# Optimization experiments

Measured on AMD Instinct MI355X. Metric: run time of the kernel, lower is better.

Reference implementation:

```python
import jax, jax.numpy as jnp
import numpy as np

B, T, D, H = 4, 4096, 1024, 64

def setup_inputs() -> dict:
    key = jax.random.key(0)
    k1, k2, k3, k4 = jax.random.split(key, 4)
    scale = 1.0 / np.sqrt(D)
    return {
        "x": jax.random.normal(k1, (B, T, D), dtype=jnp.float32),
        "Wq": jax.random.normal(k2, (D, H), dtype=jnp.float32) * scale,
        "Wk": jax.random.normal(k3, (D, H), dtype=jnp.float32) * scale,
        "Wv": jax.random.normal(k4, (D, H), dtype=jnp.float32) * scale,
    }

def reference(x, Wq, Wk, Wv):
    # Projections (Linear without bias): [B,T,H]
    q = jnp.einsum('btd,dh->bth', x, Wq)
    k = jnp.einsum('btd,dh->bth', x, Wk)
    v = jnp.einsum('btd,dh->bth', x, Wv)
    head_size = q.shape[-1]
    # Full T x T scores, scaled by sqrt(head_size) as in the source
    attn = jnp.einsum('bqh,bkh->bqk', q, k) / jnp.sqrt(jnp.float32(head_size))
    t = x.shape[1]
    causal = jnp.tril(jnp.ones((t, t), dtype=bool))  # [T,T]
    attn = jnp.where(causal[None, :, :], attn, -jnp.inf)
    attn = jax.nn.softmax(attn, axis=-1)
    # dropout prob = 0.0 -> identity
    out = jnp.einsum('bqk,bkh->bqh', attn, v)
    return out
```

## Files before the change

kernel.cpp:

```cpp
#include <hip/hip_runtime.h>
#include <hip/hip_bf16.h>
#include <math.h>

#define BB 4
#define TT 4096
#define DD 1024
#define HH 64
#define MTOT (BB * TT)
#define NCH 4

typedef short short8 __attribute__((ext_vector_type(8)));
typedef float f32x4  __attribute__((ext_vector_type(4)));
typedef unsigned int u32;
typedef unsigned long long u64;

__device__ __forceinline__ unsigned short f2bf(float f) {
    unsigned u = __builtin_bit_cast(unsigned, f);
    unsigned r = (u + 0x7fffu + ((u >> 16) & 1u)) >> 16;
    return (unsigned short)r;
}

__device__ __forceinline__ unsigned long long pack4(float a, float b, float c, float d) {
    return (unsigned long long)f2bf(a) |
           ((unsigned long long)f2bf(b) << 16) |
           ((unsigned long long)f2bf(c) << 32) |
           ((unsigned long long)f2bf(d) << 48);
}

__device__ __forceinline__ short8 pack8(float4 a, float4 b) {
    short8 r;
    r[0] = (short)f2bf(a.x); r[1] = (short)f2bf(a.y);
    r[2] = (short)f2bf(a.z); r[3] = (short)f2bf(a.w);
    r[4] = (short)f2bf(b.x); r[5] = (short)f2bf(b.y);
    r[6] = (short)f2bf(b.z); r[7] = (short)f2bf(b.w);
    return r;
}

__device__ __forceinline__ void gl16(const void* g, void* l) {
    __builtin_amdgcn_global_load_lds(
        (const __attribute__((address_space(1))) u32*)g,
        (__attribute__((address_space(3))) u32*)l, 16, 0, 0);
}

#define QOFF  0
#define KOFF  (MTOT * HH)
#define VOFF  (2 * MTOT * HH)
#define BF_TOTAL (3 * MTOT * HH)

__global__ __launch_bounds__(256) void transpose_w(
    const float* __restrict__ Wq, const float* __restrict__ Wk,
    const float* __restrict__ Wv, unsigned short* __restrict__ Wt)
{
    const int w = blockIdx.y;
    const float* W = (w == 0) ? Wq : (w == 1) ? Wk : Wv;
    unsigned short* o = Wt + (size_t)w * 64 * 1024;
    const int t  = threadIdx.x;
    const int n4 = t & 15;
    const int k0 = blockIdx.x * 64 + (t >> 4) * 4;

    float v[4][4];
#pragma unroll
    for (int ii = 0; ii < 4; ++ii) {
        float4 r = *(const float4*)&W[(size_t)(k0 + ii) * HH + n4 * 4];
        v[ii][0] = r.x; v[ii][1] = r.y; v[ii][2] = r.z; v[ii][3] = r.w;
    }
#pragma unroll
    for (int cc = 0; cc < 4; ++cc) {
        unsigned long long pk = pack4(v[0][cc], v[1][cc], v[2][cc], v[3][cc]);
        *(unsigned long long*)&o[(size_t)(n4 * 4 + cc) * 1024 + k0] = pk;
    }
}

__global__ __launch_bounds__(256, 2) void qkv_proj(
    const float* __restrict__ x,
    const unsigned short* __restrict__ Wt,
    unsigned short* __restrict__ qkv)
{
    const int tid   = threadIdx.x;
    const int lane  = tid & 63;
    const int wave  = tid >> 6;
    const int l15   = lane & 15;
    const int quad  = lane >> 4;
    const int m0    = blockIdx.x * 32;
    const int strip = wave & 1;
    const int half  = wave >> 1;

    __shared__ float          Af[2][32 * 64];
    __shared__ unsigned short Bs[2][192 * 64];

    const int ar  = lane >> 4;
    const int as  = lane & 15;
    const int bc  = lane >> 3;
    const int bs2 = (lane & 7) ^ bc;

#define STAGEW(it, p)                                                        \
    {                                                                        \
        const int kc_ = (it) * 64;                                           \
        _Pragma("unroll")                                                    \
        for (int jj = 0; jj < 2; ++jj) {                                     \
            int j   = wave * 2 + jj;                                         \
            int row = 4 * j + ar;                                            \
            int sw  = as ^ (row & 15);                                       \
            gl16(x + (size_t)(m0 + row) * DD + kc_ + sw * 4,                 \
                 &Af[p][j * 256]);                                           \
        }                                                                    \
        _Pragma("unroll")                                                    \
        for (int jj = 0; jj < 6; ++jj) {                                     \
            int j    = wave * 6 + jj;                                        \
            int gcol = 8 * j + bc;                                           \
            gl16(Wt + (size_t)gcol * 1024 + kc_ + bs2 * 8,                   \
                 &Bs[p][j * 512]);                                           \
        }                                                                    \
    }

    f32x4 acc[6];
#pragma unroll
    for (int i = 0; i < 6; ++i) acc[i] = (f32x4){0.f, 0.f, 0.f, 0.f};

    STAGEW(0, 0)
    __syncthreads();
    int p = 0;

    for (int it = 0; it < 16; ++it) {
        if (it < 15) STAGEW(it + 1, p ^ 1)

        const int row = strip * 16 + l15;
#pragma unroll
        for (int ks = 0; ks < 2; ++ks) {
            int c0 = ks * 8 + quad * 2;
            float4 a0 = *(const float4*)&Af[p][row * 64 + ((c0)     ^ l15) * 4];
            float4 a1 = *(const float4*)&Af[p][row * 64 + ((c0 + 1) ^ l15) * 4];
            short8 af = pack8(a0, a1);
            int cb = (ks * 4 + quad) ^ (l15 & 7);
#pragma unroll
            for (int jj = 0; jj < 6; ++jj) {
                int col = (half * 6 + jj) * 16 + l15;
                short8 bfr = *(const short8*)&Bs[p][col * 64 + cb * 8];
                acc[jj] = __builtin_amdgcn_mfma_f32_16x16x32_bf16(af, bfr, acc[jj], 0, 0, 0);
            }
        }
        __syncthreads();
        p ^= 1;
    }
#undef STAGEW

    const float QS = 0.125f * 1.44269504088896f;
    unsigned short* q_bf  = qkv + QOFF;
    unsigned short* k_bf  = qkv + KOFF;
    unsigned short* vt_bf = qkv + VOFF;
#pragma unroll
    for (int jj = 0; jj < 6; ++jj) {
        int g = half * 6 + jj, w = g >> 2, col = (g & 3) * 16 + l15;
#pragma unroll
        for (int r = 0; r < 4; ++r) {
            int m = m0 + strip * 16 + quad * 4 + r;
            float val = acc[jj][r];
            if (w == 0) val *= QS;
            unsigned short bv = f2bf(val);
            if (w == 0)      q_bf[(size_t)m * HH + col] = bv;
            else if (w == 1) k_bf[(size_t)m * HH + col] = bv;
            else {
                int b = m >> 12, t = m & 4095;
                vt_bf[(size_t)b * HH * TT + (size_t)col * TT + t] = bv;
            }
        }
    }
}

__global__ __launch_bounds__(256, 3) void flash_attn(
    const unsigned short* __restrict__ qkv,
    float* __restrict__ Opart,
    float* __restrict__ Mpart,
    float* __restrict__ Lpart)
{
    const int qt = 63 - blockIdx.x;
    const int b  = blockIdx.y;
    const int c  = blockIdx.z;
    if (c * 16 > qt) return;
    const int j0   = c * 16;
    const int jmax = min(j0 + 16, qt + 1);

    const int tid  = threadIdx.x;
    const int lane = tid & 63;
    const int wave = tid >> 6;
    const int l15  = lane & 15;
    const int quad = lane >> 4;

    const unsigned short* q_g  = qkv + QOFF + (size_t)b * TT * HH;
    const unsigned short* k_g  = qkv + KOFF + (size_t)b * TT * HH;
    const unsigned short* vt_g = qkv + VOFF + (size_t)b * HH * TT;

    __shared__ unsigned short Ks[2][128 * 64];
    __shared__ unsigned short Vs[64 * 128];

    const int kr3 = lane >> 3;
    const int kch = lane & 7;
    const int vr2 = lane >> 4;
    const int vch = lane & 15;

#define STAGE_K(jr_, p_)                                                      \
    {                                                                         \
        const unsigned short* kp = k_g + (size_t)(jr_) * 64 * HH;             \
        _Pragma("unroll")                                                     \
        for (int i = 0; i < 4; ++i) {                                         \
            int g = wave * 4 + i;                                             \
            gl16(kp + (size_t)(g * 8 + kr3) * HH + (kch ^ kr3) * 8,           \
                 &Ks[p_][g * 512]);                                           \
        }                                                                     \
    }
#define STAGE_V(jr_)                                                          \
    {                                                                         \
        const unsigned short* vp = vt_g + (size_t)(jr_) * 64;                 \
        _Pragma("unroll")                                                     \
        for (int i = 0; i < 4; ++i) {                                         \
            int g = wave * 4 + i;                                             \
            int h = g * 4 + vr2;                                              \
            gl16(vp + (size_t)h * TT + (vch ^ ((h >> 1) & 7)) * 8,            \
                 &Vs[g * 512]);                                               \
        }                                                                     \
    }

    short8 qf[2];
#pragma unroll
    for (int kk = 0; kk < 2; ++kk)
        qf[kk] = *(const short8*)&q_g[(size_t)(qt * 64 + wave * 16 + l15) * HH + kk * 32 + quad * 8];

    f32x4 ov[4];
#pragma unroll
    for (int i = 0; i < 4; ++i) ov[i] = (f32x4){0.f, 0.f, 0.f, 0.f};
    float m_run = -1e30f, l_run = 0.f;

    STAGE_K(j0, 0)
    __syncthreads();
    int p = 0;

    const int swv = 2 * ((l15 >> 1) & 7);

    for (int jr = j0; jr < jmax; jr += 2) {
        const bool two = (jmax - jr) >= 2;

        STAGE_V(jr)
        if (jr + 2 < jmax) STAGE_K(jr + 2, p ^ 1)

        f32x4 st0[4], st1[4];
#pragma unroll
        for (int i = 0; i < 4; ++i) {
            st0[i] = (f32x4){0.f, 0.f, 0.f, 0.f};
            st1[i] = (f32x4){0.f, 0.f, 0.f, 0.f};
        }
#pragma unroll
        for (int kk = 0; kk < 2; ++kk)
#pragma unroll
            for (int mt = 0; mt < 4; ++mt) {
                short8 a = *(const short8*)&Ks[p][(mt * 16 + l15) * 64 +
                                                  (((kk * 4 + quad) ^ (l15 & 7)) * 8)];
                st0[mt] = __builtin_amdgcn_mfma_f32_16x16x32_bf16(a, qf[kk], st0[mt], 0, 0, 0);
            }
        if (two) {
#pragma unroll
            for (int kk = 0; kk < 2; ++kk)
#pragma unroll
                for (int mt = 0; mt < 4; ++mt) {
                    short8 a = *(const short8*)&Ks[p][(64 + mt * 16 + l15) * 64 +
                                                      (((kk * 4 + quad) ^ (l15 & 7)) * 8)];
                    st1[mt] = __builtin_amdgcn_mfma_f32_16x16x32_bf16(a, qf[kk], st1[mt], 0, 0, 0);
                }
        }

        const int qg = wave * 16 + l15;
        if (jr == qt) {
#pragma unroll
            for (int mt = 0; mt < 4; ++mt)
#pragma unroll
                for (int r = 0; r < 4; ++r)
                    if (mt * 16 + quad * 4 + r > qg) st0[mt][r] = -1e30f;
        } else if (two && jr + 1 == qt) {
#pragma unroll
            for (int mt = 0; mt < 4; ++mt)
#pragma unroll
                for (int r = 0; r < 4; ++r)
                    if (mt * 16 + quad * 4 + r > qg) st1[mt][r] = -1e30f;
        }

        float mloc = -1e30f;
#pragma unroll
        for (int mt = 0; mt < 4; ++mt)
#pragma unroll
            for (int r = 0; r < 4; ++r) mloc = fmaxf(mloc, st0[mt][r]);
        if (two) {
#pragma unroll
            for (int mt = 0; mt < 4; ++mt)
#pragma unroll
                for (int r = 0; r < 4; ++r) mloc = fmaxf(mloc, st1[mt][r]);
        }
        mloc = fmaxf(mloc, __shfl_xor(mloc, 16));
        mloc = fmaxf(mloc, __shfl_xor(mloc, 32));
        const float m_new = fmaxf(m_run, mloc);
        const float alpha = exp2f(m_run - m_new);
        m_run = m_new;

        float ssum = 0.f;
#pragma unroll
        for (int mt = 0; mt < 4; ++mt)
#pragma unroll
            for (int r = 0; r < 4; ++r) {
                float pv = exp2f(st0[mt][r] - m_new);
                st0[mt][r] = pv; ssum += pv;
            }
        if (two) {
#pragma unroll
            for (int mt = 0; mt < 4; ++mt)
#pragma unroll
                for (int r = 0; r < 4; ++r) {
                    float pv = exp2f(st1[mt][r] - m_new);
                    st1[mt][r] = pv; ssum += pv;
                }
        }
        ssum += __shfl_xor(ssum, 16);
        ssum += __shfl_xor(ssum, 32);
        l_run = l_run * alpha + ssum;

        short8 pa00, pa01, pa10, pa11;
        {
            u32* pp = (u32*)&pa00;
            asm("v_cvt_pk_bf16_f32 %0, %1, %2" : "=v"(pp[0]) : "v"(st0[0][0]), "v"(st0[0][1]));
            asm("v_cvt_pk_bf16_f32 %0, %1, %2" : "=v"(pp[1]) : "v"(st0[0][2]), "v"(st0[0][3]));
            asm("v_cvt_pk_bf16_f32 %0, %1, %2" : "=v"(pp[2]) : "v"(st0[1][0]), "v"(st0[1][1]));
            asm("v_cvt_pk_bf16_f32 %0, %1, %2" : "=v"(pp[3]) : "v"(st0[1][2]), "v"(st0[1][3]));
            pp = (u32*)&pa01;
            asm("v_cvt_pk_bf16_f32 %0, %1, %2" : "=v"(pp[0]) : "v"(st0[2][0]), "v"(st0[2][1]));
            asm("v_cvt_pk_bf16_f32 %0, %1, %2" : "=v"(pp[1]) : "v"(st0[2][2]), "v"(st0[2][3]));
            asm("v_cvt_pk_bf16_f32 %0, %1, %2" : "=v"(pp[2]) : "v"(st0[3][0]), "v"(st0[3][1]));
            asm("v_cvt_pk_bf16_f32 %0, %1, %2" : "=v"(pp[3]) : "v"(st0[3][2]), "v"(st0[3][3]));
        }
        if (two) {
            u32* pp = (u32*)&pa10;
            asm("v_cvt_pk_bf16_f32 %0, %1, %2" : "=v"(pp[0]) : "v"(st1[0][0]), "v"(st1[0][1]));
            asm("v_cvt_pk_bf16_f32 %0, %1, %2" : "=v"(pp[1]) : "v"(st1[0][2]), "v"(st1[0][3]));
            asm("v_cvt_pk_bf16_f32 %0, %1, %2" : "=v"(pp[2]) : "v"(st1[1][0]), "v"(st1[1][1]));
            asm("v_cvt_pk_bf16_f32 %0, %1, %2" : "=v"(pp[3]) : "v"(st1[1][2]), "v"(st1[1][3]));
            pp = (u32*)&pa11;
            asm("v_cvt_pk_bf16_f32 %0, %1, %2" : "=v"(pp[0]) : "v"(st1[2][0]), "v"(st1[2][1]));
            asm("v_cvt_pk_bf16_f32 %0, %1, %2" : "=v"(pp[1]) : "v"(st1[2][2]), "v"(st1[2][3]));
            asm("v_cvt_pk_bf16_f32 %0, %1, %2" : "=v"(pp[2]) : "v"(st1[3][0]), "v"(st1[3][1]));
            asm("v_cvt_pk_bf16_f32 %0, %1, %2" : "=v"(pp[3]) : "v"(st1[3][2]), "v"(st1[3][3]));
        }

        {
            float a0 = __shfl(alpha, quad * 4 + 0);
            float a1 = __shfl(alpha, quad * 4 + 1);
            float a2 = __shfl(alpha, quad * 4 + 2);
            float a3 = __shfl(alpha, quad * 4 + 3);
#pragma unroll
            for (int ht = 0; ht < 4; ++ht) {
                ov[ht][0] *= a0; ov[ht][1] *= a1;
                ov[ht][2] *= a2; ov[ht][3] *= a3;
            }
        }

        __syncthreads();

#pragma unroll
        for (int kk = 0; kk < 2; ++kk) {
            short8 a = kk ? pa01 : pa00;
            int c8 = kk * 8 + quad;
#pragma unroll
            for (int ht = 0; ht < 4; ++ht) {
                int rb = (ht * 16 + l15) * 128;
                u64 lo = *(const u64*)&Vs[rb + ((c8 ^ swv) << 2)];
                u64 hi = *(const u64*)&Vs[rb + ((c8 ^ 4 ^ swv) << 2)];
                short8 vb;
                ((u64*)&vb)[0] = lo;
                ((u64*)&vb)[1] = hi;
                ov[ht] = __builtin_amdgcn_mfma_f32_16x16x32_bf16(a, vb, ov[ht], 0, 0, 0);
            }
        }
        if (two) {
#pragma unroll
            for (int kk = 0; kk < 2; ++kk) {
                short8 a = kk ? pa11 : pa10;
                int c8 = 16 + kk * 8 + quad;
#pragma unroll
                for (int ht = 0; ht < 4; ++ht) {
                    int rb = (ht * 16 + l15) * 128;
                    u64 lo = *(const u64*)&Vs[rb + ((c8 ^ swv) << 2)];
                    u64 hi = *(const u64*)&Vs[rb + ((c8 ^ 4 ^ swv) << 2)];
                    short8 vb;
                    ((u64*)&vb)[0] = lo;
                    ((u64*)&vb)[1] = hi;
                    ov[ht] = __builtin_amdgcn_mfma_f32_16x16x32_bf16(a, vb, ov[ht], 0, 0, 0);
                }
            }
        }

        __syncthreads();
        p ^= 1;
    }
#undef STAGE_K
#undef STAGE_V

    float* Ob = Opart + ((size_t)((b * 64 + qt) * NCH + c)) * 4096;
#pragma unroll
    for (int ht = 0; ht < 4; ++ht)
#pragma unroll
        for (int r = 0; r < 4; ++r)
            Ob[(size_t)(wave * 16 + quad * 4 + r) * HH + ht * 16 + l15] = ov[ht][r];
    if (quad == 0) {
        size_t mi = (size_t)((b * 64 + qt) * NCH + c) * 64 + wave * 16 + l15;
        Mpart[mi] = m_run;
        Lpart[mi] = l_run;
    }
}

__global__ __launch_bounds__(256) void combine(
    const float* __restrict__ Opart,
    const float* __restrict__ Mpart,
    const float* __restrict__ Lpart,
    float* __restrict__ out)
{
    const int qt = blockIdx.x;
    const int b  = blockIdx.y;
    const int nc = (qt >> 4) + 1;
    const int t  = threadIdx.x;
    const int row = t >> 2;
    const int seg = t & 3;

    const size_t base = (size_t)(b * 64 + qt) * NCH;

    float m_c[NCH], M = -1e30f;
    for (int c = 0; c < nc; ++c) {
        m_c[c] = Mpart[(base + c) * 64 + row];
        M = fmaxf(M, m_c[c]);
    }
    float L = 0.f, w_c[NCH];
    for (int c = 0; c < nc; ++c) {
        w_c[c] = exp2f(m_c[c] - M);
        L += w_c[c] * Lpart[(base + c) * 64 + row];
    }
    float invL = 1.0f / L;

    f32x4 o[4];
#pragma unroll
    for (int i = 0; i < 4; ++i) o[i] = (f32x4){0.f, 0.f, 0.f, 0.f};
    for (int c = 0; c < nc; ++c) {
        const float* Ob = Opart + (base + c) * 4096 + (size_t)row * HH + seg * 16;
#pragma unroll
        for (int i = 0; i < 4; ++i) {
            f32x4 v = *(const f32x4*)(Ob + i * 4);
            o[i] += v * w_c[c];
        }
    }
    float* op = out + ((size_t)b * TT + qt * 64 + row) * HH + seg * 16;
#pragma unroll
    for (int i = 0; i < 4; ++i)
        *(f32x4*)(op + i * 4) = o[i] * invL;
}

extern "C" void kernel_launch(void* const* d_in, const int* in_sizes, int n_in,
                              void* d_out, int out_size, void* d_ws, size_t ws_size,
                              hipStream_t stream) {
    const float* x  = (const float*)d_in[0];
    const float* Wq = (const float*)d_in[1];
    const float* Wk = (const float*)d_in[2];
    const float* Wv = (const float*)d_in[3];
    float* out = (float*)d_out;

    unsigned short* qkv = (unsigned short*)d_ws;
    float* Opart = (float*)((char*)d_ws + BF_TOTAL * 2);
    float* Mpart = Opart + (size_t)BB * 64 * NCH * 4096;
    float* Lpart = Mpart + (size_t)BB * 64 * NCH * 64;

    unsigned short* Wt = (unsigned short*)d_out;

    transpose_w<<<dim3(16, 3), 256, 0, stream>>>(Wq, Wk, Wv, Wt);
    qkv_proj<<<dim3(MTOT / 32), 256, 0, stream>>>(x, Wt, qkv);
    flash_attn<<<dim3(64, BB, NCH), 256, 0, stream>>>(qkv, Opart, Mpart, Lpart);
    combine<<<dim3(64, BB), 256, 0, stream>>>(Opart, Mpart, Lpart, out);
}
```

Baseline: 154.9 us.

## Skip rescale when max unchanged, use packed bf16 cvt, add MFMA setprio

Several unrelated tweaks land together. The projection kernel now converts its A fragment to bf16 with the hardware packed convert instruction instead of software rounding. The attention loop raises wave priority around its MFMA blocks and skips the alpha rescale of the output accumulator and l when no row max grows in the wave. The combine kernel is restructured to drop its local arrays. The conditional rescale saves ALU work and shuffles but adds a wave-wide vote and a branch.

```diff
diff --git a/kernel.cpp b/kernel.cpp
--- a/kernel.cpp
+++ b/kernel.cpp
@@ -25,15 +25,6 @@
            ((unsigned long long)f2bf(b) << 16) |
            ((unsigned long long)f2bf(c) << 32) |
            ((unsigned long long)f2bf(d) << 48);
-}
-
-__device__ __forceinline__ short8 pack8(float4 a, float4 b) {
-    short8 r;
-    r[0] = (short)f2bf(a.x); r[1] = (short)f2bf(a.y);
-    r[2] = (short)f2bf(a.z); r[3] = (short)f2bf(a.w);
-    r[4] = (short)f2bf(b.x); r[5] = (short)f2bf(b.y);
-    r[6] = (short)f2bf(b.z); r[7] = (short)f2bf(b.w);
-    return r;
 }
 
 __device__ __forceinline__ void gl16(const void* g, void* l) {
@@ -130,7 +121,14 @@
             int c0 = ks * 8 + quad * 2;
             float4 a0 = *(const float4*)&Af[p][row * 64 + ((c0)     ^ l15) * 4];
             float4 a1 = *(const float4*)&Af[p][row * 64 + ((c0 + 1) ^ l15) * 4];
-            short8 af = pack8(a0, a1);
+            short8 af;
+            {
+                u32* ap = (u32*)&af;
+                asm("v_cvt_pk_bf16_f32 %0, %1, %2" : "=v"(ap[0]) : "v"(a0.x), "v"(a0.y));
+                asm("v_cvt_pk_bf16_f32 %0, %1, %2" : "=v"(ap[1]) : "v"(a0.z), "v"(a0.w));
+                asm("v_cvt_pk_bf16_f32 %0, %1, %2" : "=v"(ap[2]) : "v"(a1.x), "v"(a1.y));
+                asm("v_cvt_pk_bf16_f32 %0, %1, %2" : "=v"(ap[3]) : "v"(a1.z), "v"(a1.w));
+            }
             int cb = (ks * 4 + quad) ^ (l15 & 7);
 #pragma unroll
             for (int jj = 0; jj < 6; ++jj) {
@@ -248,6 +246,7 @@
             st0[i] = (f32x4){0.f, 0.f, 0.f, 0.f};
             st1[i] = (f32x4){0.f, 0.f, 0.f, 0.f};
         }
+        __builtin_amdgcn_s_setprio(1);
 #pragma unroll
         for (int kk = 0; kk < 2; ++kk)
 #pragma unroll
@@ -266,6 +265,7 @@
                     st1[mt] = __builtin_amdgcn_mfma_f32_16x16x32_bf16(a, qf[kk], st1[mt], 0, 0, 0);
                 }
         }
+        __builtin_amdgcn_s_setprio(0);
 
         const int qg = wave * 16 + l15;
         if (jr == qt) {
@@ -295,16 +295,29 @@
         }
         mloc = fmaxf(mloc, __shfl_xor(mloc, 16));
         mloc = fmaxf(mloc, __shfl_xor(mloc, 32));
-        const float m_new = fmaxf(m_run, mloc);
-        const float alpha = exp2f(m_run - m_new);
-        m_run = m_new;
+
+        if (!__all(mloc <= m_run)) {
+            const float m_new = fmaxf(m_run, mloc);
+            const float alpha = exp2f(m_run - m_new);
+            m_run = m_new;
+            l_run *= alpha;
+            float a0 = __shfl(alpha, quad * 4 + 0);
+            float a1 = __shfl(alpha, quad * 4 + 1);
+            float a2 = __shfl(alpha, quad * 4 + 2);
+            float a3 = __shfl(alpha, quad * 4 + 3);
+#pragma unroll
+            for (int ht = 0; ht < 4; ++ht) {
+                ov[ht][0] *= a0; ov[ht][1] *= a1;
+                ov[ht][2] *= a2; ov[ht][3] *= a3;
+            }
+        }
 
         float ssum = 0.f;
 #pragma unroll
         for (int mt = 0; mt < 4; ++mt)
 #pragma unroll
             for (int r = 0; r < 4; ++r) {
-                float pv = exp2f(st0[mt][r] - m_new);
+                float pv = exp2f(st0[mt][r] - m_run);
                 st0[mt][r] = pv; ssum += pv;
             }
         if (two) {
@@ -312,13 +325,13 @@
             for (int mt = 0; mt < 4; ++mt)
 #pragma unroll
                 for (int r = 0; r < 4; ++r) {
-                    float pv = exp2f(st1[mt][r] - m_new);
+                    float pv = exp2f(st1[mt][r] - m_run);
                     st1[mt][r] = pv; ssum += pv;
                 }
         }
         ssum += __shfl_xor(ssum, 16);
         ssum += __shfl_xor(ssum, 32);
-        l_run = l_run * alpha + ssum;
+        l_run += ssum;
 
         short8 pa00, pa01, pa10, pa11;
         {
@@ -346,20 +359,9 @@
             asm("v_cvt_pk_bf16_f32 %0, %1, %2" : "=v"(pp[3]) : "v"(st1[3][2]), "v"(st1[3][3]));
         }
 
-        {
-            float a0 = __shfl(alpha, quad * 4 + 0);
-            float a1 = __shfl(alpha, quad * 4 + 1);
-            float a2 = __shfl(alpha, quad * 4 + 2);
-            float a3 = __shfl(alpha, quad * 4 + 3);
-#pragma unroll
-            for (int ht = 0; ht < 4; ++ht) {
-                ov[ht][0] *= a0; ov[ht][1] *= a1;
-                ov[ht][2] *= a2; ov[ht][3] *= a3;
-            }
-        }
-
         __syncthreads();
 
+        __builtin_amdgcn_s_setprio(1);
 #pragma unroll
         for (int kk = 0; kk < 2; ++kk) {
             short8 a = kk ? pa01 : pa00;
@@ -392,6 +394,7 @@
                 }
             }
         }
+        __builtin_amdgcn_s_setprio(0);
 
         __syncthreads();
         p ^= 1;
@@ -427,29 +430,25 @@
 
     const size_t base = (size_t)(b * 64 + qt) * NCH;
 
-    float m_c[NCH], M = -1e30f;
-    for (int c = 0; c < nc; ++c) {
-        m_c[c] = Mpart[(base + c) * 64 + row];
-        M = fmaxf(M, m_c[c]);
-    }
-    float L = 0.f, w_c[NCH];
-    for (int c = 0; c < nc; ++c) {
-        w_c[c] = exp2f(m_c[c] - M);
-        L += w_c[c] * Lpart[(base + c) * 64 + row];
-    }
-    float invL = 1.0f / L;
-
+    float M = -1e30f;
+    for (int c = 0; c < nc; ++c)
+        M = fmaxf(M, Mpart[(base + c) * 64 + row]);
+
+    float L = 0.f;
     f32x4 o[4];
 #pragma unroll
     for (int i = 0; i < 4; ++i) o[i] = (f32x4){0.f, 0.f, 0.f, 0.f};
     for (int c = 0; c < nc; ++c) {
+        float w = exp2f(Mpart[(base + c) * 64 + row] - M);
+        L += w * Lpart[(base + c) * 64 + row];
         const float* Ob = Opart + (base + c) * 4096 + (size_t)row * HH + seg * 16;
 #pragma unroll
         for (int i = 0; i < 4; ++i) {
             f32x4 v = *(const f32x4*)(Ob + i * 4);
-            o[i] += v * w_c[c];
-        }
-    }
+            o[i] += v * w;
+        }
+    }
+    float invL = 1.0f / L;
     float* op = out + ((size_t)b * TT + qt * 64 + row) * HH + seg * 16;
 #pragma unroll
     for (int i = 0; i < 4; ++i)
```

Measured after the change: 152.6 us. Within noise of the previous version (-1.5%).
